# Kernel optimization log

Measured on AMD Instinct MI355X. Metric: run time of the kernel, lower is better.

Reference implementation:

```python
import jax, jax.numpy as jnp
import numpy as np

GAMMA = 2.0
ALPHA = jnp.array([0.25, 0.75], dtype=jnp.float32)  # [neg, pos]
MAX_CLUTTER = 39
PROTECTED = 2
HARD_NUM = round(MAX_CLUTTER * (1.0 / 4.0))  # 10
EASY_NUM = MAX_CLUTTER - HARD_NUM            # 29
TOPK = 200


def setup_inputs() -> dict:
    key = jax.random.key(0)
    k1, k2 = jax.random.split(key)
    b, t, h, w = 8, 16, 512, 512
    x = jax.random.normal(k1, (b, t, h, w), dtype=jnp.float32)
    target = (jax.random.uniform(k2, (b, t, h, w)) > 0.999).astype(jnp.int32)
    return {"x": x, "target": target}


def _protected_mask(tgt_f):
    # conv3d with an all-ones (1, 5, 5) kernel followed by (>0) is equivalent
    # to "any positive in the 5x5 spatial window" since tgt_f is 0/1.
    win = 2 * PROTECTED + 1
    m = jax.lax.reduce_window(tgt_f, -jnp.inf, jax.lax.max,
                              (1, 1, win, win), (1, 1, 1, 1), 'SAME')
    return (m > 0).astype(tgt_f.dtype)


def reference(x, target):
    b, t, h, w = x.shape
    tgt = target.astype(jnp.float32)
    prot = _protected_mask(tgt)                      # [b,t,h,w]

    logpt = jax.nn.log_sigmoid(x)
    logpt_bk = jax.nn.log_sigmoid(-x)

    # --- no-grad hard-positive-mining mask (detached in original) ---
    bce = -tgt * logpt - (1.0 - tgt) * logpt_bk       # BCEWithLogits, no reduce
    loss_p = bce * (1.0 - prot)
    loss_sum = jnp.sum(loss_p, axis=1).reshape(b, h * w)  # sum over t -> [b, hw]

    key = jax.random.key(42)
    k_idx, k_easy = jax.random.split(key)
    # idx = randperm(130) + 20 : random picks among top-[20,150) hardest pixels,
    # shared across the batch (computed once before the loop in the original)
    idx = jax.random.permutation(k_idx, 130)[:HARD_NUM] + 20
    _, top_idx = jax.lax.top_k(loss_sum, TOPK)        # [b, 200]
    hard = top_idx[:, idx]                            # [b, HARD_NUM]
    # per-sample random easy pixels (randperm(hw)[:EASY_NUM] per sample)
    easy_keys = jax.random.split(k_easy, b)
    easy = jax.vmap(lambda k: jax.random.permutation(k, h * w)[:EASY_NUM])(easy_keys)
    sel = jnp.concatenate([hard, easy], axis=1)       # [b, 39]

    mask2d = jnp.zeros((b, h * w), jnp.float32)
    mask2d = mask2d.at[jnp.arange(b)[:, None], sel].set(1.0)
    wgt = mask2d.reshape(b, 1, h, w)                  # broadcasts over t

    wgt_new = wgt * (1.0 - prot) + tgt
    wgt_new = (wgt_new > 0).astype(jnp.float32)
    wgt_new = jax.lax.stop_gradient(wgt_new)

    # --- focal loss (pt, pt_bk are .data i.e. detached) ---
    pt = jax.lax.stop_gradient(jnp.exp(logpt))
    pt_bk = jax.lax.stop_gradient(1.0 - jnp.exp(logpt_bk))
    loss = (-ALPHA[1] * (1.0 - pt) ** GAMMA * tgt * logpt
            - ALPHA[0] * pt_bk ** GAMMA * (1.0 - tgt) * logpt_bk)
    return jnp.sum(loss * wgt_new)
```

## Files before the change

kernel.cpp:

```cpp
#include <hip/hip_runtime.h>
#include <cstdint>
#include <vector>
#include <algorithm>
#include <utility>

#define BN 8
#define TN 16
#define HN 512
#define WN 512
#define HWN (HN*WN)
#define HARDN 10
#define EASYN 29
#define NSEL 39
#define NBIN 4096
#define CAP 2048

typedef unsigned long long u64;

static const size_t LS_OFF   = 0;
static const size_t HIST_OFF = LS_OFF + (size_t)BN*HWN*4;
static const size_t CCNT_OFF = HIST_OFF + (size_t)BN*NBIN*4;
static const size_t CAND_OFF = CCNT_OFF + 64;
static const size_t SEL_OFF  = CAND_OFF + (size_t)BN*CAP*8;
static const size_t ACC_OFF  = SEL_OFF + (size_t)BN*64*4;

struct SelConst { int idxpos[HARDN]; int easy[BN][EASYN]; };

#define JAX_PARTITIONABLE 1

static inline void tf2x32(uint32_t k0, uint32_t k1, uint32_t& x0, uint32_t& x1) {
  uint32_t ks0 = k0, ks1 = k1, ks2 = k0 ^ k1 ^ 0x1BD11BDAu;
  uint32_t v0 = x0 + ks0, v1 = x1 + ks1;
  static const int r0[4] = {13,15,26,6}, r1[4] = {17,29,16,24};
  uint32_t ks[3] = {ks0, ks1, ks2};
  for (int i = 0; i < 5; ++i) {
    const int* rot = (i & 1) ? r1 : r0;
    for (int j = 0; j < 4; ++j) {
      v0 += v1;
      v1 = (v1 << rot[j]) | (v1 >> (32 - rot[j]));
      v1 ^= v0;
    }
    v0 += ks[(i + 1) % 3];
    v1 += ks[(i + 2) % 3] + (uint32_t)(i + 1);
  }
  x0 = v0; x1 = v1;
}

static void jax_split(uint32_t k0, uint32_t k1, int num, uint32_t* out) {
#if JAX_PARTITIONABLE
  for (int j = 0; j < num; ++j) {
    uint32_t a = 0, b = (uint32_t)j;
    tf2x32(k0, k1, a, b);
    out[2*j] = a; out[2*j+1] = b;
  }
#else
  int h = num;
  std::vector<uint32_t> o(2*num);
  for (int i = 0; i < h; ++i) {
    uint32_t a = (uint32_t)i, b = (uint32_t)(i + h);
    tf2x32(k0, k1, a, b);
    o[i] = a; o[i+h] = b;
  }
  for (int i = 0; i < 2*num; ++i) out[i] = o[i];
#endif
}

static void jax_bits(uint32_t k0, uint32_t k1, uint32_t n, std::vector<uint32_t>& bits) {
  bits.resize(n);
#if JAX_PARTITIONABLE
  for (uint32_t i = 0; i < n; ++i) {
    uint32_t a = 0, b = i;
    tf2x32(k0, k1, a, b);
    bits[i] = a ^ b;
  }
#else
  uint32_t h = n / 2;
  for (uint32_t i = 0; i < h; ++i) {
    uint32_t a = i, b = i + h;
    tf2x32(k0, k1, a, b);
    bits[i] = a; bits[i+h] = b;
  }
#endif
}

static void jax_shuffle(uint32_t k0, uint32_t k1, std::vector<uint32_t>& x, int rounds) {
  size_t n = x.size();
  std::vector<uint32_t> bits;
  std::vector<std::pair<uint64_t,uint32_t>> tmp(n);
  uint32_t ck0 = k0, ck1 = k1;
  for (int r = 0; r < rounds; ++r) {
    uint32_t sp[4];
    jax_split(ck0, ck1, 2, sp);
    ck0 = sp[0]; ck1 = sp[1];
    jax_bits(sp[2], sp[3], (uint32_t)n, bits);
    for (size_t i = 0; i < n; ++i)
      tmp[i] = { ((uint64_t)bits[i] << 32) | (uint32_t)i, x[i] };
    std::sort(tmp.begin(), tmp.end(),
              [](const std::pair<uint64_t,uint32_t>& A,
                 const std::pair<uint64_t,uint32_t>& B){ return A.first < B.first; });
    for (size_t i = 0; i < n; ++i) x[i] = tmp[i].second;
  }
}

static SelConst build_sel() {
  SelConst sc;
  uint32_t root[4];
  jax_split(0u, 42u, 2, root);
  {
    std::vector<uint32_t> x(130);
    for (int i = 0; i < 130; ++i) x[i] = (uint32_t)i;
    jax_shuffle(root[0], root[1], x, 1);
    for (int j = 0; j < HARDN; ++j) sc.idxpos[j] = (int)x[j] + 20;
  }
  uint32_t ek[2*BN];
  jax_split(root[2], root[3], BN, ek);
  for (int b = 0; b < BN; ++b) {
    std::vector<uint32_t> x(HWN);
    for (uint32_t i = 0; i < (uint32_t)HWN; ++i) x[i] = i;
    jax_shuffle(ek[2*b], ek[2*b+1], x, 2);
    for (int j = 0; j < EASYN; ++j) sc.easy[b][j] = (int)x[j];
  }
  return sc;
}

static const SelConst g_sc = build_sel();

__global__ __launch_bounds__(256) void kInit(unsigned int* __restrict__ hist,
                                             unsigned int* __restrict__ ccnt,
                                             double* __restrict__ accum) {
  int i = blockIdx.x * 256 + threadIdx.x;
  if (i < BN*NBIN) hist[i] = 0u;
  if (i < BN) ccnt[i] = 0u;
  if (i == 0) *accum = 0.0;
}

__global__ __launch_bounds__(256) void kA(const float* __restrict__ x,
                                          const int* __restrict__ tgt,
                                          float* __restrict__ loss_sum,
                                          double* __restrict__ accum) {
  const int tile = blockIdx.x;
  const int b    = blockIdx.y;
  const int ty = (tile >> 3) << 4;
  const int tx = (tile & 7) << 6;
  const int tid = threadIdx.x;
  const int c = tid & 63;
  const int w = tid >> 6;

  __shared__ u64 Mbuf[2][20];
  __shared__ u64 Hbuf[2][20];
  __shared__ double s_pos[4];

  float lsum[4] = {0.f, 0.f, 0.f, 0.f};
  double posA = 0.0;

#define PHASE1(T, PB) do {                                                      \
    const int* tg_ = tgt + (((size_t)(b*TN + (T))) << 18);                      \
    for (int r = w; r < 20; r += 4) {                                           \
      int gy = ty + r - 2; int tv = 0, hv = 0;                                  \
      if ((unsigned)gy < (unsigned)HN) {                                        \
        const int* rowp = tg_ + (gy << 9);                                      \
        tv = rowp[tx + c];                                                      \
        if (c < 2)        { int gx = tx - 2 + c; if (gx >= 0) hv = rowp[gx]; }  \
        else if (c >= 62) { int gx = tx + 2 + c; if (gx < WN) hv = rowp[gx]; }  \
      }                                                                         \
      u64 mb = __ballot(tv > 0);                                                \
      u64 hb = __ballot(hv > 0);                                                \
             \
      u64 lo = (hb & 3ull) | (mb << 2);                                         \
      u64 hi = (mb >> 62) | (((hb >> 62) & 3ull) << 2);                         \
      u64 Hv = lo | (lo >> 1) | (lo >> 2) | (lo >> 3) | (lo >> 4)               \
                  | (hi << 63) | (hi << 62) | (hi << 61) | (hi << 60);          \
      if (c == 0) { Mbuf[PB][r] = mb; Hbuf[PB][r] = Hv; }                       \
    }                                                                           \
  } while (0)

  PHASE1(0, 0);
  __syncthreads();

  for (int t = 0; t < TN; ++t) {
    const int pb = t & 1;
    {
      const float* xx = x + (((size_t)(b*TN + t)) << 18);
      const int rb = 4 * w;
      u64 h0 = Hbuf[pb][rb+0], h1 = Hbuf[pb][rb+1], h2 = Hbuf[pb][rb+2],
          h3 = Hbuf[pb][rb+3], h4 = Hbuf[pb][rb+4], h5 = Hbuf[pb][rb+5],
          h6 = Hbuf[pb][rb+6], h7 = Hbuf[pb][rb+7];
      u64 t23 = h2 | h3, t45 = h4 | h5;
      u64 Ps[4];
      Ps[0] = h0 | h1 | t23 | h4;
      Ps[1] = h1 | t23 | t45;
      Ps[2] = t23 | t45 | h6;
      Ps[3] = h3 | t45 | h6 | h7;
      u64 Ms[4] = {Mbuf[pb][rb+2], Mbuf[pb][rb+3], Mbuf[pb][rb+4], Mbuf[pb][rb+5]};
      #pragma unroll
      for (int i = 0; i < 4; ++i) {
        float xv = xx[((ty + rb + i) << 9) + tx + c];
        unsigned tvb   = (unsigned)((Ms[i] >> c) & 1ull);
        unsigned protb = (unsigned)((Ps[i] >> c) & 1ull);
        float l1p = log1pf(expf(-fabsf(xv)));
        float bce = fmaxf(tvb ? -xv : xv, 0.f) + l1p;
        if (!protb) lsum[i] += bce;
        if (Ms[i]) {
          if (tvb) {
            float logpt = -bce;
            float pt = expf(logpt);
            float om = 1.f - pt;
            posA += (double)(-0.75f * om * om * logpt);
          }
        }
      }
    }
    if (t + 1 < TN) PHASE1(t + 1, (t + 1) & 1);
    __syncthreads();
  }
#undef PHASE1

  float* ls = loss_sum + (((size_t)b) << 18);
  {
    const int rb = 4 * w;
    #pragma unroll
    for (int i = 0; i < 4; ++i)
      ls[((ty + rb + i) << 9) + tx + c] = lsum[i];
  }

  for (int off = 32; off > 0; off >>= 1) posA += __shfl_down(posA, off, 64);
  if (c == 0) s_pos[w] = posA;
  __syncthreads();
  if (tid == 0)
    atomicAdd(accum, s_pos[0] + s_pos[1] + s_pos[2] + s_pos[3]);
}

__global__ __launch_bounds__(256) void kHist(const float* __restrict__ loss_sum,
                                             unsigned int* __restrict__ hist) {
  const int part = blockIdx.x;
  const int row  = blockIdx.y;
  const int tid  = threadIdx.x;
  __shared__ unsigned int sh[NBIN];
  for (int i = tid; i < NBIN; i += 256) sh[i] = 0u;
  __syncthreads();
  const float4* ls4 = (const float4*)(loss_sum + (((size_t)row) << 18) + part*(HWN/64));
  #pragma unroll
  for (int i = 0; i < 4; ++i) {
    float4 v = ls4[tid + 256*i];
    atomicAdd(&sh[__float_as_uint(v.x) >> 19], 1u);
    atomicAdd(&sh[__float_as_uint(v.y) >> 19], 1u);
    atomicAdd(&sh[__float_as_uint(v.z) >> 19], 1u);
    atomicAdd(&sh[__float_as_uint(v.w) >> 19], 1u);
  }
  __syncthreads();
  unsigned int* gh = hist + (row << 12);
  for (int i = tid; i < NBIN; i += 256) {
    unsigned int cc = sh[i];
    if (cc) atomicAdd(&gh[i], cc);
  }
}

__global__ __launch_bounds__(256) void kCollect(const float* __restrict__ loss_sum,
                                                const unsigned int* __restrict__ hist,
                                                unsigned int* __restrict__ ccnt,
                                                unsigned long long* __restrict__ cand) {
  const int part = blockIdx.x;
  const int row  = blockIdx.y;
  const int tid  = threadIdx.x;
  __shared__ unsigned int s_chunk[256];
  __shared__ int s_thr;
  const unsigned int* gh = hist + (row << 12);
  unsigned int cs = 0;
  #pragma unroll
  for (int j = 0; j < 16; ++j) cs += gh[tid*16 + j];
  s_chunk[tid] = cs;
  __syncthreads();
  if (tid == 0) {
    int thr = 0;
    unsigned int cum = 0;
    for (int c = 255; c >= 0; --c) {
      unsigned int cc = s_chunk[c];
      if (cum + cc >= 200u) {
        unsigned int cum2 = cum;
        int bin;
        for (bin = c*16 + 15; bin > c*16; --bin) {
          cum2 += gh[bin];
          if (cum2 >= 200u) break;
        }
        thr = bin;
        break;
      }
      cum += cc;
    }
    s_thr = thr;
  }
  __syncthreads();
  const int thr = s_thr;
  const float* ls = loss_sum + (((size_t)row) << 18);
  unsigned long long* cr = cand + (size_t)row * CAP;
  const int lo = part * (HWN/64), hi = lo + (HWN/64);
  for (int i = lo + tid; i < hi; i += 256) {
    unsigned int vb = __float_as_uint(ls[i]);
    if ((int)(vb >> 19) >= thr) {
      unsigned int pos = atomicAdd(&ccnt[row], 1u);
      if (pos < CAP)
        cr[pos] = (((unsigned long long)(~vb)) << 32) | (unsigned int)i;
    }
  }
}

__global__ __launch_bounds__(1024) void kSelect(const unsigned long long* __restrict__ cand,
                                                const unsigned int* __restrict__ ccnt,
                                                int* __restrict__ sel, SelConst sc) {
  const int row = blockIdx.x;
  const int tid = threadIdx.x;
  __shared__ u64 s_k[CAP];
  __shared__ int s_hard[HARDN];
  unsigned int nu = ccnt[row]; if (nu > CAP) nu = CAP;
  const int n = (int)nu;
  const u64* cr = cand + (size_t)row * CAP;
  for (int i = tid; i < n; i += 1024) s_k[i] = cr[i];
  __syncthreads();
  for (int ci = tid; ci < n; ci += 1024) {
    u64 my = s_k[ci];
    int rank = 0;
    for (int j = 0; j < n; ++j) rank += (s_k[j] < my) ? 1 : 0;
    #pragma unroll
    for (int h = 0; h < HARDN; ++h)
      if (rank == sc.idxpos[h]) s_hard[h] = (int)(unsigned int)(my & 0xFFFFFFFFULL);
  }
  __syncthreads();
  if (tid < NSEL) {
    int v;
    if (tid < HARDN) {
      v = s_hard[tid];
    } else {
      int e = sc.easy[row][tid - HARDN];
      bool dup = false;
      #pragma unroll
      for (int j = 0; j < HARDN; ++j) dup |= (s_hard[j] == e);
      v = dup ? -1 : e;
    }
    sel[row*64 + tid] = v;
  }
}

__global__ __launch_bounds__(128) void kC(const float* __restrict__ x,
                                          const int* __restrict__ tgt,
                                          const int* __restrict__ sel,
                                          double* __restrict__ accum) {
  const int si  = blockIdx.x;
  const int row = blockIdx.y;
  const int p = sel[row*64 + si];
  if (p < 0) return;
  const int cy = p >> 9, cx = p & 511;
  const int tid = threadIdx.x;
  const int t = tid >> 3, sub = tid & 7;
  const size_t base = ((size_t)(row*TN + t)) << 18;
  const int* tg = tgt + base;
  int protc = 0;
  for (int w = sub; w < 25; w += 8) {
    int dy = w / 5 - 2, dx = w % 5 - 2;
    int gy = cy + dy, gx = cx + dx;
    if ((unsigned)gy < (unsigned)HN && (unsigned)gx < (unsigned)WN)
      protc += tg[(gy << 9) + gx];
  }
  protc += __shfl_xor(protc, 1, 64);
  protc += __shfl_xor(protc, 2, 64);
  protc += __shfl_xor(protc, 4, 64);
  __shared__ double s_term[TN];
  if (sub == 0) {
    double term = 0.0;
    int tv = tg[(cy << 9) + cx];
    if (tv == 0 && protc == 0) {
      float xv = x[base + (size_t)((cy << 9) + cx)];
      float l1p = log1pf(expf(-fabsf(xv)));
      float logptbk = -(fmaxf(xv, 0.f) + l1p);
      float ptbk = 1.f - expf(logptbk);
      term = (double)(-0.25f * ptbk * ptbk * logptbk);
    }
    s_term[t] = term;
  }
  __syncthreads();
  if (tid == 0) {
    double s = 0.0;
    #pragma unroll
    for (int u = 0; u < TN; ++u) s += s_term[u];
    atomicAdd(accum, s);
  }
}

__global__ void kD(const double* __restrict__ accum, float* __restrict__ out) {
  out[0] = (float)(*accum);
}

extern "C" void kernel_launch(void* const* d_in, const int* in_sizes, int n_in,
                              void* d_out, int out_size, void* d_ws, size_t ws_size,
                              hipStream_t stream) {
  const float* x   = (const float*)d_in[0];
  const int*   tgt = (const int*)d_in[1];
  float* out = (float*)d_out;
  char* ws = (char*)d_ws;
  float*              loss_sum = (float*)(ws + LS_OFF);
  unsigned int*       hist     = (unsigned int*)(ws + HIST_OFF);
  unsigned int*       ccnt     = (unsigned int*)(ws + CCNT_OFF);
  unsigned long long* cand     = (unsigned long long*)(ws + CAND_OFF);
  int*                sel      = (int*)(ws + SEL_OFF);
  double*             accum    = (double*)(ws + ACC_OFF);

  hipLaunchKernelGGL(kInit,    dim3((BN*NBIN + 255)/256), dim3(256), 0, stream, hist, ccnt, accum);
  hipLaunchKernelGGL(kA,       dim3(256, BN), dim3(256),  0, stream, x, tgt, loss_sum, accum);
  hipLaunchKernelGGL(kHist,    dim3(64, BN),  dim3(256),  0, stream, loss_sum, hist);
  hipLaunchKernelGGL(kCollect, dim3(64, BN),  dim3(256),  0, stream, loss_sum, hist, ccnt, cand);
  hipLaunchKernelGGL(kSelect,  dim3(BN),      dim3(1024), 0, stream, cand, ccnt, sel, g_sc);
  hipLaunchKernelGGL(kC,       dim3(NSEL, BN),dim3(128),  0, stream, x, tgt, sel, accum);
  hipLaunchKernelGGL(kD,       dim3(1),       dim3(1),    0, stream, accum, out);
}
```

Before: 475.3 us.

## Fuse histogram into main pass and compute 5x5 mask per wave without LDS

Folds the separate loss-sum histogram kernel into the main pass: each block builds a shared-memory histogram of its own loss sums, aggregating equal bins within a wave via ballot, then flushes to the global histogram. It also drops the double-buffered shared bitmask staging and per-timestep block barriers. Each wave now loads its own 8 target rows (including halo) per timestep and builds the protected mask from register ballots. This removes a kernel launch, a reread of loss_sum, and per-step syncs, at the cost of redundant halo loads and 16KB of LDS per block, which may lower occupancy.

```diff
diff --git a/kernel.cpp b/kernel.cpp
--- a/kernel.cpp
+++ b/kernel.cpp
@@ -137,6 +137,7 @@
 __global__ __launch_bounds__(256) void kA(const float* __restrict__ x,
                                           const int* __restrict__ tgt,
                                           float* __restrict__ loss_sum,
+                                          unsigned int* __restrict__ hist,
                                           double* __restrict__ accum) {
   const int tile = blockIdx.x;
   const int b    = blockIdx.y;
@@ -145,114 +146,105 @@
   const int tid = threadIdx.x;
   const int c = tid & 63;
   const int w = tid >> 6;
-
-  __shared__ u64 Mbuf[2][20];
-  __shared__ u64 Hbuf[2][20];
+  const int r0g = ty + 4*w - 2;
+
+  __shared__ unsigned int sh[NBIN];
   __shared__ double s_pos[4];
+
+  for (int i = tid; i < NBIN; i += 256) sh[i] = 0u;
+  __syncthreads();
 
   float lsum[4] = {0.f, 0.f, 0.f, 0.f};
   double posA = 0.0;
 
-#define PHASE1(T, PB) do {                                                      \
-    const int* tg_ = tgt + (((size_t)(b*TN + (T))) << 18);                      \
-    for (int r = w; r < 20; r += 4) {                                           \
-      int gy = ty + r - 2; int tv = 0, hv = 0;                                  \
-      if ((unsigned)gy < (unsigned)HN) {                                        \
-        const int* rowp = tg_ + (gy << 9);                                      \
-        tv = rowp[tx + c];                                                      \
-        if (c < 2)        { int gx = tx - 2 + c; if (gx >= 0) hv = rowp[gx]; }  \
-        else if (c >= 62) { int gx = tx + 2 + c; if (gx < WN) hv = rowp[gx]; }  \
-      }                                                                         \
-      u64 mb = __ballot(tv > 0);                                                \
-      u64 hb = __ballot(hv > 0);                                                \
-             \
-      u64 lo = (hb & 3ull) | (mb << 2);                                         \
-      u64 hi = (mb >> 62) | (((hb >> 62) & 3ull) << 2);                         \
-      u64 Hv = lo | (lo >> 1) | (lo >> 2) | (lo >> 3) | (lo >> 4)               \
-                  | (hi << 63) | (hi << 62) | (hi << 61) | (hi << 60);          \
-      if (c == 0) { Mbuf[PB][r] = mb; Hbuf[PB][r] = Hv; }                       \
-    }                                                                           \
-  } while (0)
-
-  PHASE1(0, 0);
-  __syncthreads();
+  const int gxh = (c < 2) ? (tx - 2 + c) : ((c >= 62) ? (tx + 2 + c) : -1);
+  const bool hvalid = ((unsigned)gxh < (unsigned)WN);
 
   for (int t = 0; t < TN; ++t) {
-    const int pb = t & 1;
-    {
-      const float* xx = x + (((size_t)(b*TN + t)) << 18);
-      const int rb = 4 * w;
-      u64 h0 = Hbuf[pb][rb+0], h1 = Hbuf[pb][rb+1], h2 = Hbuf[pb][rb+2],
-          h3 = Hbuf[pb][rb+3], h4 = Hbuf[pb][rb+4], h5 = Hbuf[pb][rb+5],
-          h6 = Hbuf[pb][rb+6], h7 = Hbuf[pb][rb+7];
-      u64 t23 = h2 | h3, t45 = h4 | h5;
-      u64 Ps[4];
-      Ps[0] = h0 | h1 | t23 | h4;
-      Ps[1] = h1 | t23 | t45;
-      Ps[2] = t23 | t45 | h6;
-      Ps[3] = h3 | t45 | h6 | h7;
-      u64 Ms[4] = {Mbuf[pb][rb+2], Mbuf[pb][rb+3], Mbuf[pb][rb+4], Mbuf[pb][rb+5]};
-      #pragma unroll
-      for (int i = 0; i < 4; ++i) {
-        float xv = xx[((ty + rb + i) << 9) + tx + c];
-        unsigned tvb   = (unsigned)((Ms[i] >> c) & 1ull);
-        unsigned protb = (unsigned)((Ps[i] >> c) & 1ull);
-        float l1p = log1pf(expf(-fabsf(xv)));
-        float bce = fmaxf(tvb ? -xv : xv, 0.f) + l1p;
-        if (!protb) lsum[i] += bce;
-        if (Ms[i]) {
-          if (tvb) {
-            float logpt = -bce;
-            float pt = expf(logpt);
-            float om = 1.f - pt;
-            posA += (double)(-0.75f * om * om * logpt);
-          }
+    const size_t base = ((size_t)(b*TN + t)) << 18;
+    const int*   tg = tgt + base;
+    const float* xx = x   + base;
+
+    int tvv[8], hvv[8];
+    #pragma unroll
+    for (int r = 0; r < 8; ++r) {
+      const int gy = r0g + r;
+      const bool rv = ((unsigned)gy < (unsigned)HN);
+      const int* rowp = tg + ((size_t)gy << 9);
+      tvv[r] = rv ? rowp[tx + c] : 0;
+      hvv[r] = (rv && hvalid) ? rowp[gxh] : 0;
+    }
+    float xv[4];
+    #pragma unroll
+    for (int i = 0; i < 4; ++i)
+      xv[i] = xx[((size_t)(r0g + 2 + i) << 9) + tx + c];
+
+    u64 m[8], H[8];
+    #pragma unroll
+    for (int r = 0; r < 8; ++r) {
+      u64 mb = __ballot(tvv[r] > 0);
+      u64 hb = __ballot(hvv[r] > 0);
+      u64 lo = (hb & 3ull) | (mb << 2);
+      u64 hi = (mb >> 62) | (((hb >> 62) & 3ull) << 2);
+      m[r] = mb;
+      H[r] = lo | (lo >> 1) | (lo >> 2) | (lo >> 3) | (lo >> 4)
+           | (hi << 63) | (hi << 62) | (hi << 61) | (hi << 60);
+    }
+    const u64 t23 = H[2] | H[3], t45 = H[4] | H[5];
+    u64 Ps[4];
+    Ps[0] = H[0] | H[1] | t23 | H[4];
+    Ps[1] = H[1] | t23 | t45;
+    Ps[2] = t23 | t45 | H[6];
+    Ps[3] = H[3] | t45 | H[6] | H[7];
+
+    #pragma unroll
+    for (int i = 0; i < 4; ++i) {
+      const float xvi = xv[i];
+      const unsigned tvb   = (unsigned)((m[i+2] >> c) & 1ull);
+      const unsigned protb = (unsigned)((Ps[i]  >> c) & 1ull);
+      const float l1p = log1pf(expf(-fabsf(xvi)));
+      const float bce = fmaxf(tvb ? -xvi : xvi, 0.f) + l1p;
+      if (!protb) lsum[i] += bce;
+      if (m[i+2]) {
+        if (tvb) {
+          const float logpt = -bce;
+          const float pt = expf(logpt);
+          const float om = 1.f - pt;
+          posA += (double)(-0.75f * om * om * logpt);
         }
       }
     }
-    if (t + 1 < TN) PHASE1(t + 1, (t + 1) & 1);
-    __syncthreads();
-  }
-#undef PHASE1
+  }
 
   float* ls = loss_sum + (((size_t)b) << 18);
-  {
-    const int rb = 4 * w;
-    #pragma unroll
-    for (int i = 0; i < 4; ++i)
-      ls[((ty + rb + i) << 9) + tx + c] = lsum[i];
+  #pragma unroll
+  for (int i = 0; i < 4; ++i)
+    ls[((size_t)(r0g + 2 + i) << 9) + tx + c] = lsum[i];
+
+  #pragma unroll
+  for (int i = 0; i < 4; ++i) {
+    const unsigned bin = __float_as_uint(lsum[i]) >> 19;
+    u64 active = ~0ull;
+    while (active) {
+      const int lead = (int)(__ffsll((unsigned long long)active) - 1);
+      const unsigned lbin = (unsigned)__shfl((int)bin, lead, 64);
+      const u64 same = __ballot(bin == lbin);
+      if (c == lead) atomicAdd(&sh[lbin], (unsigned)__popcll(same));
+      active &= ~same;
+    }
   }
 
   for (int off = 32; off > 0; off >>= 1) posA += __shfl_down(posA, off, 64);
   if (c == 0) s_pos[w] = posA;
   __syncthreads();
+
+  unsigned int* gh = hist + (b << 12);
+  for (int i = tid; i < NBIN; i += 256) {
+    const unsigned cc = sh[i];
+    if (cc) atomicAdd(&gh[i], cc);
+  }
   if (tid == 0)
     atomicAdd(accum, s_pos[0] + s_pos[1] + s_pos[2] + s_pos[3]);
-}
-
-__global__ __launch_bounds__(256) void kHist(const float* __restrict__ loss_sum,
-                                             unsigned int* __restrict__ hist) {
-  const int part = blockIdx.x;
-  const int row  = blockIdx.y;
-  const int tid  = threadIdx.x;
-  __shared__ unsigned int sh[NBIN];
-  for (int i = tid; i < NBIN; i += 256) sh[i] = 0u;
-  __syncthreads();
-  const float4* ls4 = (const float4*)(loss_sum + (((size_t)row) << 18) + part*(HWN/64));
-  #pragma unroll
-  for (int i = 0; i < 4; ++i) {
-    float4 v = ls4[tid + 256*i];
-    atomicAdd(&sh[__float_as_uint(v.x) >> 19], 1u);
-    atomicAdd(&sh[__float_as_uint(v.y) >> 19], 1u);
-    atomicAdd(&sh[__float_as_uint(v.z) >> 19], 1u);
-    atomicAdd(&sh[__float_as_uint(v.w) >> 19], 1u);
-  }
-  __syncthreads();
-  unsigned int* gh = hist + (row << 12);
-  for (int i = tid; i < NBIN; i += 256) {
-    unsigned int cc = sh[i];
-    if (cc) atomicAdd(&gh[i], cc);
-  }
 }
 
 __global__ __launch_bounds__(256) void kCollect(const float* __restrict__ loss_sum,
@@ -404,8 +396,7 @@
   double*             accum    = (double*)(ws + ACC_OFF);
 
   hipLaunchKernelGGL(kInit,    dim3((BN*NBIN + 255)/256), dim3(256), 0, stream, hist, ccnt, accum);
-  hipLaunchKernelGGL(kA,       dim3(256, BN), dim3(256),  0, stream, x, tgt, loss_sum, accum);
-  hipLaunchKernelGGL(kHist,    dim3(64, BN),  dim3(256),  0, stream, loss_sum, hist);
+  hipLaunchKernelGGL(kA,       dim3(256, BN), dim3(256),  0, stream, x, tgt, loss_sum, hist, accum);
   hipLaunchKernelGGL(kCollect, dim3(64, BN),  dim3(256),  0, stream, loss_sum, hist, ccnt, cand);
   hipLaunchKernelGGL(kSelect,  dim3(BN),      dim3(1024), 0, stream, cand, ccnt, sel, g_sc);
   hipLaunchKernelGGL(kC,       dim3(NSEL, BN),dim3(128),  0, stream, x, tgt, sel, accum);
```

Measured after the change: 451.6 us. 5.0% less time.
